# Kernel tuning notes

Hardware: AMD Instinct MI355X
Metric: run time of the kernel (lower is better)

## Reference

```python
import jax, jax.numpy as jnp
import numpy as np

EPS = 1e-5


def setup_inputs() -> dict:
    key = jax.random.key(0)
    ks = jax.random.split(key, 12)
    B, S, M, D, H, dh = 8, 512, 512, 1024, 16, 64
    T = S + M
    w_scale = 0.03  # keep attention logits in a sane range (mimics nn.Linear init scale)
    return {
        "x": jax.random.normal(ks[0], (B, S, D), jnp.float32),
        "mem": jax.random.normal(ks[1], (B, M, D), jnp.float32),
        "R": jax.random.normal(ks[2], (T, D), jnp.float32),
        "u": jax.random.normal(ks[3], (1, H, 1, dh), jnp.float32) * 0.1,
        "t": jax.random.normal(ks[4], (1, H, 1, dh), jnp.float32) * 0.1,
        "Wq": jax.random.normal(ks[5], (H * dh, D), jnp.float32) * w_scale,
        "Wk": jax.random.normal(ks[6], (H * dh, D), jnp.float32) * w_scale,
        "Wv": jax.random.normal(ks[7], (H * dh, D), jnp.float32) * w_scale,
        "Wr": jax.random.normal(ks[8], (H * dh, D), jnp.float32) * w_scale,
        "Wo": jax.random.normal(ks[9], (D, H * dh), jnp.float32) * w_scale,
        "gamma": jnp.ones((D,), jnp.float32),
        "beta": jnp.zeros((D,), jnp.float32),
    }


def reference(x, mem, R, u, t, Wq, Wk, Wv, Wr, Wo, gamma, beta):
    B, S, D = x.shape
    H, dh = u.shape[1], u.shape[3]
    h = jnp.concatenate([mem, x], axis=1)          # [B, T, D]
    T = h.shape[1]
    M = T - S

    q = (x @ Wq.T).reshape(B, S, H, dh).transpose(0, 2, 1, 3)   # [B,H,S,dh]
    k = (h @ Wk.T).reshape(B, T, H, dh).transpose(0, 2, 1, 3)   # [B,H,T,dh]
    v = (h @ Wv.T).reshape(B, T, H, dh).transpose(0, 2, 1, 3)   # [B,H,T,dh]
    r = (R[-T:] @ Wr.T).reshape(1, T, H, dh).transpose(0, 2, 1, 3)  # [1,H,T,dh]

    ac = jnp.einsum("bhid,bhjd->bhij", q + u, k)                # [B,H,S,T]
    bd = jnp.einsum("bhid,hjd->bhij", q + t, r[0])              # [B,H,S,T]

    # circulant shift: shifted[..., i, j] = bd[..., i, (j - i + S - 1) % T]
    idx = (jnp.arange(T)[None, :] - jnp.arange(S)[:, None] + S - 1) % T  # [S,T]
    bd = jnp.take_along_axis(bd, idx[None, None], axis=3)

    # causal mask with memory offset: keep j <= i + M (tril(mem_len)), then
    # exact-zero entries (the masked ones) become -inf, matching the original.
    mask = jnp.arange(T)[None, :] <= (jnp.arange(S)[:, None] + M)        # [S,T]
    score = jnp.where(mask[None, None], (ac + bd) / jnp.sqrt(jnp.float32(dh)), 0.0)
    score = jnp.where(score == 0, -jnp.inf, score)
    p = jax.nn.softmax(score, axis=-1)                                   # [B,H,S,T]

    att = jnp.einsum("bhij,bhjd->bhid", p, v).transpose(0, 2, 1, 3).reshape(B, S, H * dh)
    out = att @ Wo.T                                                      # dropout is identity (p=0/eval)

    y = out + x
    mu = jnp.mean(y, axis=-1, keepdims=True)
    var = jnp.var(y, axis=-1, keepdims=True)
    return (y - mu) / jnp.sqrt(var + EPS) * gamma + beta
```

## Files before the change

### kernel.cpp

```cpp
#include <hip/hip_runtime.h>
#include <math.h>

#define BB 8
#define SS 512
#define MM 512
#define TT 1024
#define DD 1024
#define HH 16
#define DH 64

typedef __attribute__((ext_vector_type(8))) short bf16x8;
typedef __attribute__((ext_vector_type(4))) float f32x4;

#define SCL2E 0.1803368801111f
#define DTHR 11.5f

__device__ __forceinline__ ushort f2bf(float f) {
  union { float f; unsigned u; } x; x.f = f;
  unsigned r = x.u + 0x7fffu + ((x.u >> 16) & 1u);
  return (ushort)(r >> 16);
}
__device__ __forceinline__ float bf2f(ushort u) {
  return __builtin_bit_cast(float, ((unsigned)u) << 16);
}

__device__ __forceinline__ void stage16(void* lds, const void* g) {
  __builtin_amdgcn_global_load_lds((const __attribute__((address_space(1))) void*)g,
                                   (__attribute__((address_space(3))) void*)lds, 16, 0, 0);
}

template <int C>
__device__ __forceinline__ float dppf(float x) {
  return __builtin_bit_cast(float,
      __builtin_amdgcn_update_dpp(0, __builtin_bit_cast(int, x), C, 0xF, 0xF, true));
}
__device__ __forceinline__ float redmax16(float x) {
  x = fmaxf(x, dppf<0xB1>(x));
  x = fmaxf(x, dppf<0x4E>(x));
  x = fmaxf(x, dppf<0x141>(x));
  x = fmaxf(x, dppf<0x140>(x));
  return x;
}
__device__ __forceinline__ float redsum16(float x) {
  x += dppf<0xB1>(x);
  x += dppf<0x4E>(x);
  x += dppf<0x141>(x);
  x += dppf<0x140>(x);
  return x;
}
__device__ __forceinline__ float bperm_f(int byteaddr, float v) {
  return __builtin_bit_cast(float,
      __builtin_amdgcn_ds_bpermute(byteaddr, __builtin_bit_cast(int, v)));
}

__global__ __launch_bounds__(256) void cast_all(
    const float* __restrict__ mem, const float* __restrict__ x,
    const float* __restrict__ R, const float* __restrict__ Wq,
    const float* __restrict__ Wk, const float* __restrict__ Wv,
    const float* __restrict__ Wr, const float* __restrict__ Wo,
    ushort* __restrict__ hb, ushort* __restrict__ Rb, ushort* __restrict__ Wqb,
    ushort* __restrict__ Wkb, ushort* __restrict__ Wvb, ushort* __restrict__ Wrb,
    ushort* __restrict__ Wob) {
  const int M1 = 1 << 20;
  int i = (blockIdx.x * 256 + threadIdx.x) * 8;
  const float* src;
  ushort* dst;
  if (i < 4 * M1) {
    src = mem + i;
    dst = hb + (size_t)i + (size_t)(i >> 19) * 524288;
  } else if (i < 8 * M1) {
    int j = i - 4 * M1;
    src = x + j;
    dst = hb + (size_t)j + (size_t)(j >> 19) * 524288 + 524288;
  } else if (i < 9 * M1) {
    src = R + (i - 8 * M1);  dst = Rb + (i - 8 * M1);
  } else if (i < 10 * M1) {
    src = Wq + (i - 9 * M1); dst = Wqb + (i - 9 * M1);
  } else if (i < 11 * M1) {
    src = Wk + (i - 10 * M1); dst = Wkb + (i - 10 * M1);
  } else if (i < 12 * M1) {
    src = Wv + (i - 11 * M1); dst = Wvb + (i - 11 * M1);
  } else if (i < 13 * M1) {
    src = Wr + (i - 12 * M1); dst = Wrb + (i - 12 * M1);
  } else {
    src = Wo + (i - 13 * M1); dst = Wob + (i - 13 * M1);
  }
  float4 a = *(const float4*)(src);
  float4 c = *(const float4*)(src + 4);
  union { bf16x8 v; ushort u[8]; } pk;
  pk.u[0] = f2bf(a.x); pk.u[1] = f2bf(a.y); pk.u[2] = f2bf(a.z); pk.u[3] = f2bf(a.w);
  pk.u[4] = f2bf(c.x); pk.u[5] = f2bf(c.y); pk.u[6] = f2bf(c.z); pk.u[7] = f2bf(c.w);
  *(bf16x8*)(void*)dst = pk.v;
}

__global__ __launch_bounds__(256, 4) void gemm_qkvr(
    const ushort* __restrict__ hb, const ushort* __restrict__ Rbuf,
    const ushort* __restrict__ Wqb, const ushort* __restrict__ Wkb,
    const ushort* __restrict__ Wvb, const ushort* __restrict__ Wrb,
    ushort* __restrict__ qub,
    ushort* __restrict__ kbo, ushort* __restrict__ vtb, ushort* __restrict__ rbo,
    const float* __restrict__ uvec) {
  __shared__ ushort As0[4096], Bs0[4096], As1[4096], Bs1[4096];
  const int bid = (blockIdx.x & 7) * 168 + (blockIdx.x >> 3);
  const ushort* A;
  const ushort* W;
  ushort* C0 = nullptr;
  bool qadd = false, qslice = false, vmode = false;
  int mt, nx;
  if (bid < 256) {
    mt = bid >> 3; nx = bid & 7;
    A = hb; W = Wqb; C0 = qub; qadd = true; qslice = true;
  } else if (bid < 768) {
    int r = bid - 256; mt = r >> 3; nx = r & 7;
    A = hb; W = Wkb; C0 = kbo;
  } else if (bid < 1280) {
    int r = bid - 768; mt = r >> 3; nx = r & 7;
    A = hb; W = Wvb; C0 = vtb; vmode = true;
  } else {
    int r = bid - 1280; mt = r >> 3; nx = r & 7;
    A = Rbuf; W = Wrb; C0 = rbo;
  }
  const int m0 = mt * 128, n0 = nx * 128;

  const int t = threadIdx.x;
  const int w = t >> 6, l = t & 63;
  const int m16 = l & 15, kg = l >> 4;
  const int wr = w >> 1, wc = w & 1;

  const int c0 = t, c1 = t + 256;
  const int scol = (((t & 3) ^ ((t >> 3) & 3)) * 8);
  const ushort* asrc0;
  const ushort* asrc1;
  {
    int gm0 = m0 + (c0 >> 2), gm1 = m0 + (c1 >> 2);
    if (qslice) {
      asrc0 = A + ((size_t)((gm0 >> 9) * TT + MM + (gm0 & 511))) * DD + scol;
      asrc1 = A + ((size_t)((gm1 >> 9) * TT + MM + (gm1 & 511))) * DD + scol;
    } else {
      asrc0 = A + (size_t)gm0 * DD + scol;
      asrc1 = A + (size_t)gm1 * DD + scol;
    }
  }
  const ushort* bsrc0 = W + (size_t)(n0 + (c0 >> 2)) * DD + scol;
  const ushort* bsrc1 = W + (size_t)(n0 + (c1 >> 2)) * DD + scol;

  const int cbx = ((kg ^ ((m16 >> 1) & 3)) << 3);
  const int arow0 = (wr * 64 + m16) * 32 + cbx;
  const int brow0 = (wc * 64 + m16) * 32 + cbx;

  f32x4 acc[4][4];
#pragma unroll
  for (int mi = 0; mi < 4; ++mi)
#pragma unroll
    for (int ni = 0; ni < 4; ++ni) acc[mi][ni] = (f32x4){0.f, 0.f, 0.f, 0.f};

#define QKVR_STAGE(AS, BS, KOFF)                \
  do {                                          \
    stage16(AS + c0 * 8, asrc0 + (KOFF));       \
    stage16(AS + c1 * 8, asrc1 + (KOFF));       \
    stage16(BS + c0 * 8, bsrc0 + (KOFF));       \
    stage16(BS + c1 * 8, bsrc1 + (KOFF));       \
  } while (0)

#define QKVR_COMPUTE(AS, BS)                                                      \
  do {                                                                            \
    bf16x8 af[4], bfr[4];                                                         \
    _Pragma("unroll") for (int mi = 0; mi < 4; ++mi)                              \
        af[mi] = *(const bf16x8*)(const void*)&AS[arow0 + mi * 512];              \
    _Pragma("unroll") for (int ni = 0; ni < 4; ++ni)                              \
        bfr[ni] = *(const bf16x8*)(const void*)&BS[brow0 + ni * 512];             \
    _Pragma("unroll") for (int mi = 0; mi < 4; ++mi)                              \
        _Pragma("unroll") for (int ni = 0; ni < 4; ++ni)                          \
            acc[mi][ni] = __builtin_amdgcn_mfma_f32_16x16x32_bf16(                \
                af[mi], bfr[ni], acc[mi][ni], 0, 0, 0);                           \
  } while (0)

  QKVR_STAGE(As0, Bs0, 0);

#pragma unroll 1
  for (int kt = 0; kt < 32; kt += 2) {
    QKVR_STAGE(As1, Bs1, (kt + 1) << 5);
    asm volatile("s_waitcnt vmcnt(4)" ::: "memory");
    __builtin_amdgcn_s_barrier();
    QKVR_COMPUTE(As0, Bs0);
    __builtin_amdgcn_s_barrier();
    if (kt + 2 < 32) {
      QKVR_STAGE(As0, Bs0, (kt + 2) << 5);
      asm volatile("s_waitcnt vmcnt(4)" ::: "memory");
    } else {
      asm volatile("s_waitcnt vmcnt(0)" ::: "memory");
    }
    __builtin_amdgcn_s_barrier();
    QKVR_COMPUTE(As1, Bs1);
    __builtin_amdgcn_s_barrier();
  }
#undef QKVR_STAGE
#undef QKVR_COMPUTE

  const int rbase = m0 + wr * 64 + kg * 4;
  const int cbase = n0 + wc * 64 + m16;
  if (vmode) {
    const int bb = m0 >> 10;
    const int tt0 = (m0 & 1023) + wr * 64 + kg * 4;
#pragma unroll
    for (int mi = 0; mi < 4; ++mi)
#pragma unroll
      for (int ni = 0; ni < 4; ++ni) {
        ushort4 o;
        o.x = f2bf(acc[mi][ni][0]); o.y = f2bf(acc[mi][ni][1]);
        o.z = f2bf(acc[mi][ni][2]); o.w = f2bf(acc[mi][ni][3]);
        *(ushort4*)(C0 + ((size_t)(bb * 1024 + cbase + ni * 16) << 10) + tt0 + mi * 16) = o;
      }
  } else if (qadd) {
    float uv[4];
#pragma unroll
    for (int ni = 0; ni < 4; ++ni) uv[ni] = uvec[cbase + ni * 16];
#pragma unroll
    for (int mi = 0; mi < 4; ++mi)
#pragma unroll
      for (int ni = 0; ni < 4; ++ni)
#pragma unroll
        for (int rg = 0; rg < 4; ++rg)
          C0[(size_t)(rbase + mi * 16 + rg) * DD + cbase + ni * 16] = f2bf(acc[mi][ni][rg] + uv[ni]);
  } else {
#pragma unroll
    for (int mi = 0; mi < 4; ++mi)
#pragma unroll
      for (int ni = 0; ni < 4; ++ni)
#pragma unroll
        for (int rg = 0; rg < 4; ++rg)
          C0[(size_t)(rbase + mi * 16 + rg) * DD + cbase + ni * 16] = f2bf(acc[mi][ni][rg]);
  }
}

__global__ __launch_bounds__(256) void gemm_wo(const ushort* __restrict__ A,
                                               const ushort* __restrict__ W,
                                               ushort* __restrict__ Cb) {
  __shared__ ushort As[128 * 32];
  __shared__ ushort Bs[64 * 32];
  const int bid = (blockIdx.x & 7) * 64 + (blockIdx.x >> 3);
  const int mt = bid >> 4, nxt = bid & 15;
  const int m0 = mt * 128, n0 = nxt * 64;
  const int t = threadIdx.x;
  const int w = t >> 6, l = t & 63;
  const int m16 = l & 15, kg = l >> 4;
  const int wr = w >> 1, wc = w & 1;

  const int scol = (((t & 3) ^ ((t >> 3) & 3)) * 8);
  const ushort* asrc0 = A + (size_t)(m0 + (t >> 2)) * DD + scol;
  const ushort* asrc1 = A + (size_t)(m0 + 64 + (t >> 2)) * DD + scol;
  const ushort* bsrc0 = W + (size_t)(n0 + (t >> 2)) * DD + scol;
  ushort* adst0 = As + t * 8;
  ushort* adst1 = As + (t + 256) * 8;
  ushort* bdst0 = Bs + t * 8;

  const int cbx = ((kg ^ ((m16 >> 1) & 3)) << 3);

  f32x4 acc[4][2];
#pragma unroll
  for (int mi = 0; mi < 4; ++mi)
#pragma unroll
    for (int ni = 0; ni < 2; ++ni) acc[mi][ni] = (f32x4){0.f, 0.f, 0.f, 0.f};

  for (int k0 = 0; k0 < DD; k0 += 32) {
    stage16(adst0, asrc0 + k0);
    stage16(adst1, asrc1 + k0);
    stage16(bdst0, bsrc0 + k0);
    __syncthreads();
    bf16x8 af[4], bfr[2];
#pragma unroll
    for (int mi = 0; mi < 4; ++mi)
      af[mi] = *(const bf16x8*)(const void*)&As[(wr * 64 + mi * 16 + m16) * 32 + cbx];
#pragma unroll
    for (int ni = 0; ni < 2; ++ni)
      bfr[ni] = *(const bf16x8*)(const void*)&Bs[(wc * 32 + ni * 16 + m16) * 32 + cbx];
#pragma unroll
    for (int mi = 0; mi < 4; ++mi)
#pragma unroll
      for (int ni = 0; ni < 2; ++ni)
        acc[mi][ni] = __builtin_amdgcn_mfma_f32_16x16x32_bf16(af[mi], bfr[ni], acc[mi][ni], 0, 0, 0);
    __syncthreads();
  }

  const int rbase = m0 + wr * 64 + kg * 4;
  const int cbase = n0 + wc * 32 + m16;
#pragma unroll
  for (int mi = 0; mi < 4; ++mi)
#pragma unroll
    for (int ni = 0; ni < 2; ++ni)
#pragma unroll
      for (int rg = 0; rg < 4; ++rg)
        Cb[(size_t)(rbase + mi * 16 + rg) * DD + cbase + ni * 16] = f2bf(acc[mi][ni][rg]);
}

__global__ __launch_bounds__(256) void attn_mfma(const ushort* __restrict__ qu,
                                                 const ushort* __restrict__ kb,
                                                 const ushort* __restrict__ vt,
                                                 const ushort* __restrict__ rb,
                                                 const float* __restrict__ uvec,
                                                 const float* __restrict__ tvec,
                                                 ushort* __restrict__ att) {
  const int w = threadIdx.x >> 6;
  const int l = threadIdx.x & 63;
  const int m16 = l & 15;
  const int kg = l >> 4;
  const int bid = blockIdx.x;
  const int it = 7 - (bid >> 7);
  const int bh = bid & 127;
  const int b = bh >> 4, h = bh & 15;
  const int i0 = it * 64;

  __shared__ ushort Ks[2][4096];
  __shared__ ushort Vs[4096];
  __shared__ ushort Rl[8192];
  __shared__ ushort plds[4][16][72];

  bf16x8 aqu[2], aqt[2];
  {
    const ushort* qrow = qu + ((size_t)(b * SS + i0 + w * 16 + m16)) * DD + h * DH + kg * 8;
    aqu[0] = *(const bf16x8*)(const void*)(qrow);
    aqu[1] = *(const bf16x8*)(const void*)(qrow + 32);
#pragma unroll
    for (int ks = 0; ks < 2; ++ks) {
      ushort* a = (ushort*)&aqt[ks];
      const ushort* qa = (const ushort*)&aqu[ks];
#pragma unroll
      for (int e = 0; e < 8; ++e) {
        const int col = h * DH + kg * 8 + ks * 32 + e;
        a[e] = f2bf(bf2f(qa[e]) + (tvec[col] - uvec[col]));
      }
    }
  }

  int baddr[4];
  bool bsel[4];
#pragma unroll
  for (int rg = 0; rg < 4; ++rg) {
    const int rw = kg * 4 + rg;
    baddr[rg] = (kg * 16 + ((m16 + 15 - rw) & 15)) << 2;
    bsel[rg] = m16 > rw;
  }

  const int c0 = threadIdx.x, c1 = threadIdx.x + 256;
  const int r0 = c0 >> 3, sc0 = ((c0 & 7) * 8) ^ ((r0 & 7) << 3);
  const int r1 = c1 >> 3, sc1 = ((c1 & 7) * 8) ^ ((r1 & 7) << 3);
  const ushort* kp0 = kb + ((size_t)(b * TT) + r0) * DD + h * DH + sc0;
  const ushort* kp1 = kb + ((size_t)(b * TT) + r1) * DD + h * DH + sc1;
  const ushort* vp0 = vt + ((size_t)(b * 1024 + h * DH + r0)) * 1024 + sc0;
  const ushort* vp1 = vt + ((size_t)(b * 1024 + h * DH + r1)) * 1024 + sc1;

  const int cb0 = (kg * 8) ^ ((m16 & 7) << 3);
  const int cb1 = (kg * 8 + 32) ^ ((m16 & 7) << 3);
  int slot64[5];
#pragma unroll
  for (int f = 0; f < 5; ++f)
    slot64[f] = ((496 - i0 - w * 16 + m16 + f * 16) & 127) << 6;

  {
    const int base0 = 448 - i0;
#pragma unroll
    for (int kk = 0; kk < 4; ++kk) {
      int c = threadIdx.x + kk * 256;
      int ro = c >> 3, cc = c & 7;
      int p = base0 + ro;
      int slot = p & 127;
      stage16(Rl + slot * 64 + cc * 8,
              rb + (size_t)p * DD + h * DH + ((cc * 8) ^ ((ro & 7) << 3)));
    }
  }
  stage16(&Ks[0][c0 * 8], kp0);
  stage16(&Ks[0][c1 * 8], kp1);
  stage16(Vs + c0 * 8, vp0);
  stage16(Vs + c1 * 8, vp1);
  kp0 += (size_t)64 * DD; kp1 += (size_t)64 * DD;
  vp0 += 64; vp1 += 64;

  f32x4 O[4];
  float mrow[4], lrow[4];
#pragma unroll
  for (int nt = 0; nt < 4; ++nt) O[nt] = (f32x4){0.f, 0.f, 0.f, 0.f};
#pragma unroll
  for (int rg = 0; rg < 4; ++rg) { mrow[rg] = -1e30f; lrow[rg] = 0.f; }

  const int ntj = it + 9;
  int cur = 0;
  for (int jt = 0; jt < ntj; ++jt) {
    const int j0 = jt * 64;

    if (jt > 0) {
      stage16(Vs + c0 * 8, vp0);
      stage16(Vs + c1 * 8, vp1);
      vp0 += 64; vp1 += 64;
      const int pstart = 512 + j0 - i0;
#pragma unroll
      for (int kk = 0; kk < 2; ++kk) {
        int c = threadIdx.x + kk * 256;
        int ro = c >> 3, cc = c & 7;
        int p = pstart + ro;
        int pc = p < 1023 ? p : 1023;
        int slot = p & 127;
        stage16(Rl + slot * 64 + cc * 8,
                rb + (size_t)pc * DD + h * DH + ((cc * 8) ^ ((ro & 7) << 3)));
      }
    }
    __syncthreads();

    const ushort* kbase = &Ks[cur][0];
    f32x4 ac[4];
    __builtin_amdgcn_s_setprio(1);
#pragma unroll
    for (int nt = 0; nt < 4; ++nt) {
      ac[nt] = (f32x4){0.f, 0.f, 0.f, 0.f};
      const int row = nt * 16 + m16;
#pragma unroll
      for (int ks = 0; ks < 2; ++ks) {
        bf16x8 bk = *(const bf16x8*)(const void*)(kbase + row * 64 + (ks == 0 ? cb0 : cb1));
        ac[nt] = __builtin_amdgcn_mfma_f32_16x16x32_bf16(aqu[ks], bk, ac[nt], 0, 0, 0);
      }
    }
    __builtin_amdgcn_s_setprio(0);

    if (jt + 1 < ntj) {
      stage16(&Ks[cur ^ 1][c0 * 8], kp0);
      stage16(&Ks[cur ^ 1][c1 * 8], kp1);
      kp0 += (size_t)64 * DD; kp1 += (size_t)64 * DD;
    }

    f32x4 bd[5];
    __builtin_amdgcn_s_setprio(1);
#pragma unroll
    for (int f = 0; f < 5; ++f) {
      f32x4 z = (f32x4){0.f, 0.f, 0.f, 0.f};
      bf16x8 b0 = *(const bf16x8*)(const void*)(Rl + slot64[f] + cb0);
      z = __builtin_amdgcn_mfma_f32_16x16x32_bf16(aqt[0], b0, z, 0, 0, 0);
      bf16x8 b1 = *(const bf16x8*)(const void*)(Rl + slot64[f] + cb1);
      bd[f] = __builtin_amdgcn_mfma_f32_16x16x32_bf16(aqt[1], b1, z, 0, 0, 0);
    }
    __builtin_amdgcn_s_setprio(0);
#pragma unroll
    for (int f = 0; f < 5; ++f) slot64[f] = (slot64[f] + 4096) & 8191;

    float sca[4][4];
#pragma unroll
    for (int rg = 0; rg < 4; ++rg) {
      float rr[5];
#pragma unroll
      for (int f = 0; f < 5; ++f) rr[f] = bperm_f(baddr[rg], bd[f][rg]);
#pragma unroll
      for (int nt = 0; nt < 4; ++nt) {
        float bdv = bsel[rg] ? rr[nt + 1] : rr[nt];
        sca[nt][rg] = (ac[nt][rg] + bdv) * SCL2E;
      }
    }
    if (jt == ntj - 1) {
#pragma unroll
      for (int rg = 0; rg < 4; ++rg) {
        const int jmax = i0 + w * 16 + kg * 4 + rg + MM;
#pragma unroll
        for (int nt = 0; nt < 4; ++nt)
          sca[nt][rg] = (j0 + nt * 16 + m16 <= jmax) ? sca[nt][rg] : -1e30f;
      }
    }

    float pmax[4];
#pragma unroll
    for (int rg = 0; rg < 4; ++rg) {
      float pm = fmaxf(fmaxf(sca[0][rg], sca[1][rg]), fmaxf(sca[2][rg], sca[3][rg]));
      pmax[rg] = redmax16(pm);
    }
    bool grow = false;
#pragma unroll
    for (int rg = 0; rg < 4; ++rg) grow = grow || (pmax[rg] > mrow[rg] + DTHR);
    if (__any(grow)) {
#pragma unroll
      for (int rg = 0; rg < 4; ++rg) {
        float mnew = fmaxf(mrow[rg], pmax[rg]);
        float scale = __builtin_amdgcn_exp2f(mrow[rg] - mnew);
        mrow[rg] = mnew;
        lrow[rg] *= scale;
#pragma unroll
        for (int nt = 0; nt < 4; ++nt) O[nt][rg] *= scale;
      }
    }

#pragma unroll
    for (int rg = 0; rg < 4; ++rg) {
      float ps = 0.f;
#pragma unroll
      for (int nt = 0; nt < 4; ++nt) {
        float p = __builtin_amdgcn_exp2f(sca[nt][rg] - mrow[rg]);
        ps += p;
        plds[w][kg * 4 + rg][nt * 16 + m16] = f2bf(p);
      }
      lrow[rg] += redsum16(ps);
    }

    __builtin_amdgcn_s_setprio(1);
#pragma unroll
    for (int ks = 0; ks < 2; ++ks) {
      bf16x8 pa = *(const bf16x8*)(const void*)&plds[w][m16][kg * 8 + ks * 32];
#pragma unroll
      for (int nt = 0; nt < 4; ++nt) {
        bf16x8 vf = *(const bf16x8*)(const void*)(Vs + (nt * 16 + m16) * 64 + (ks == 0 ? cb0 : cb1));
        O[nt] = __builtin_amdgcn_mfma_f32_16x16x32_bf16(pa, vf, O[nt], 0, 0, 0);
      }
    }
    __builtin_amdgcn_s_setprio(0);

    __syncthreads();
    cur ^= 1;
  }

  float linv[4];
#pragma unroll
  for (int rg = 0; rg < 4; ++rg) linv[rg] = 1.f / lrow[rg];
#pragma unroll
  for (int nt = 0; nt < 4; ++nt) {
#pragma unroll
    for (int rg = 0; rg < 4; ++rg) {
      att[((size_t)(b * SS + i0 + w * 16 + kg * 4 + rg)) * DD + h * DH + nt * 16 + m16] =
          f2bf(O[nt][rg] * linv[rg]);
    }
  }
}

__global__ __launch_bounds__(256) void ln_kernel(const ushort* __restrict__ ypre,
                                                 const ushort* __restrict__ hb,
                                                 const float* __restrict__ gamma,
                                                 const float* __restrict__ beta,
                                                 float* __restrict__ out) {
  const int row = blockIdx.x;
  const int t = threadIdx.x;
  const int lane = t & 63, w = t >> 6;
  const ushort* yr = ypre + (size_t)row * DD;
  const ushort* xr = hb + ((size_t)((row >> 9) * TT + MM + (row & 511))) * DD;

  ushort4 yv = *(const ushort4*)(yr + t * 4);
  ushort4 xv = *(const ushort4*)(xr + t * 4);
  float v0 = bf2f(yv.x) + bf2f(xv.x), v1 = bf2f(yv.y) + bf2f(xv.y);
  float v2 = bf2f(yv.z) + bf2f(xv.z), v3 = bf2f(yv.w) + bf2f(xv.w);

  float s = v0 + v1 + v2 + v3;
  float ss = v0 * v0 + v1 * v1 + v2 * v2 + v3 * v3;
  __shared__ float rs[4], rss[4];
#pragma unroll
  for (int off = 32; off; off >>= 1) {
    s += __shfl_xor(s, off);
    ss += __shfl_xor(ss, off);
  }
  if (!lane) { rs[w] = s; rss[w] = ss; }
  __syncthreads();
  s = rs[0] + rs[1] + rs[2] + rs[3];
  ss = rss[0] + rss[1] + rss[2] + rss[3];
  const float mu = s * (1.f / DD);
  const float var = ss * (1.f / DD) - mu * mu;
  const float rstd = rsqrtf(var + 1e-5f);

  float4 g = *(const float4*)(gamma + t * 4);
  float4 be = *(const float4*)(beta + t * 4);
  float4 o;
  o.x = (v0 - mu) * rstd * g.x + be.x;
  o.y = (v1 - mu) * rstd * g.y + be.y;
  o.z = (v2 - mu) * rstd * g.z + be.z;
  o.w = (v3 - mu) * rstd * g.w + be.w;
  *(float4*)(out + (size_t)row * DD + t * 4) = o;
}

extern "C" void kernel_launch(void* const* d_in, const int* in_sizes, int n_in,
                              void* d_out, int out_size, void* d_ws, size_t ws_size,
                              hipStream_t stream) {
  const float* x = (const float*)d_in[0];
  const float* mem = (const float*)d_in[1];
  const float* R = (const float*)d_in[2];
  const float* u = (const float*)d_in[3];
  const float* tv = (const float*)d_in[4];
  const float* Wq = (const float*)d_in[5];
  const float* Wk = (const float*)d_in[6];
  const float* Wv = (const float*)d_in[7];
  const float* Wr = (const float*)d_in[8];
  const float* Wo = (const float*)d_in[9];
  const float* gamma = (const float*)d_in[10];
  const float* beta = (const float*)d_in[11];
  float* out = (float*)d_out;

  ushort* hb = (ushort*)d_ws;
  ushort* Rb = hb + (8u << 20);
  ushort* Wqb = Rb + (1u << 20);
  ushort* Wkb = Wqb + (1u << 20);
  ushort* Wvb = Wkb + (1u << 20);
  ushort* Wrb = Wvb + (1u << 20);
  ushort* Wob = Wrb + (1u << 20);
  ushort* qu_b = Wob + (1u << 20);
  ushort* kb = qu_b + (4u << 20);
  ushort* vt = kb + (8u << 20);
  ushort* rb = vt + (8u << 20);
  ushort* att = qu_b;
  ushort* ypre = kb;

  dim3 blk(256);

  cast_all<<<dim3(7168), blk, 0, stream>>>(mem, x, R, Wq, Wk, Wv, Wr, Wo,
                                           hb, Rb, Wqb, Wkb, Wvb, Wrb, Wob);

  gemm_qkvr<<<dim3(1344), blk, 0, stream>>>(hb, Rb, Wqb, Wkb, Wvb, Wrb,
                                            qu_b, kb, vt, rb, u);

  attn_mfma<<<dim3(BB * HH * 8), blk, 0, stream>>>(qu_b, kb, vt, rb, u, tv, att);

  gemm_wo<<<dim3(512), blk, 0, stream>>>(att, Wob, ypre);

  ln_kernel<<<dim3(BB * SS), blk, 0, stream>>>(ypre, hb, gamma, beta, out);
}
```

Measured before the change: 162.2 us.

## Double-buffer K, V and R tiles with explicit vmcnt waits in attention

Restructures the attention loop so the K, V and R tiles for the next iteration are all prefetched into a second LDS buffer before the current tile is computed. The loop is unrolled by two to alternate buffers statically. __syncthreads is replaced by raw s_barrier plus a partial s_waitcnt vmcnt, so only the current tile's loads are awaited. The goal is to hide global-load latency behind the MFMA work. The cost is more LDS (V double-buffered, R ring doubled), which may lower occupancy, and correctness now depends on the hand-counted vmcnt value.

```diff
diff --git a/kernel.cpp b/kernel.cpp
--- a/kernel.cpp
+++ b/kernel.cpp
@@ -310,9 +310,9 @@
   const int b = bh >> 4, h = bh & 15;
   const int i0 = it * 64;
 
-  __shared__ ushort Ks[2][4096];
-  __shared__ ushort Vs[4096];
-  __shared__ ushort Rl[8192];
+  __shared__ ushort Ks0[4096], Ks1[4096];
+  __shared__ ushort Vs0[4096], Vs1[4096];
+  __shared__ ushort Rl[16384];
   __shared__ ushort plds[4][16][72];
 
   bf16x8 aqu[2], aqt[2];
@@ -354,7 +354,7 @@
   int slot64[5];
 #pragma unroll
   for (int f = 0; f < 5; ++f)
-    slot64[f] = ((496 - i0 - w * 16 + m16 + f * 16) & 127) << 6;
+    slot64[f] = ((496 - i0 - w * 16 + m16 + f * 16) & 255) << 6;
 
   {
     const int base0 = 448 - i0;
@@ -363,15 +363,15 @@
       int c = threadIdx.x + kk * 256;
       int ro = c >> 3, cc = c & 7;
       int p = base0 + ro;
-      int slot = p & 127;
+      int slot = p & 255;
       stage16(Rl + slot * 64 + cc * 8,
               rb + (size_t)p * DD + h * DH + ((cc * 8) ^ ((ro & 7) << 3)));
     }
   }
-  stage16(&Ks[0][c0 * 8], kp0);
-  stage16(&Ks[0][c1 * 8], kp1);
-  stage16(Vs + c0 * 8, vp0);
-  stage16(Vs + c1 * 8, vp1);
+  stage16(Ks0 + c0 * 8, kp0);
+  stage16(Ks0 + c1 * 8, kp1);
+  stage16(Vs0 + c0 * 8, vp0);
+  stage16(Vs0 + c1 * 8, vp1);
   kp0 += (size_t)64 * DD; kp1 += (size_t)64 * DD;
   vp0 += 64; vp1 += 64;
 
@@ -383,29 +383,29 @@
   for (int rg = 0; rg < 4; ++rg) { mrow[rg] = -1e30f; lrow[rg] = 0.f; }
 
   const int ntj = it + 9;
-  int cur = 0;
-  for (int jt = 0; jt < ntj; ++jt) {
+
+  auto stage_next = [&](ushort* KN, ushort* VN, int jt) {
+    stage16(KN + c0 * 8, kp0);
+    stage16(KN + c1 * 8, kp1);
+    kp0 += (size_t)64 * DD; kp1 += (size_t)64 * DD;
+    stage16(VN + c0 * 8, vp0);
+    stage16(VN + c1 * 8, vp1);
+    vp0 += 64; vp1 += 64;
+    const int pstart = 576 + jt * 64 - i0;
+#pragma unroll
+    for (int kk = 0; kk < 2; ++kk) {
+      int c = threadIdx.x + kk * 256;
+      int ro = c >> 3, cc = c & 7;
+      int p = pstart + ro;
+      int pc = p < 1023 ? p : 1023;
+      int slot = p & 255;
+      stage16(Rl + slot * 64 + cc * 8,
+              rb + (size_t)pc * DD + h * DH + ((cc * 8) ^ ((ro & 7) << 3)));
+    }
+  };
+
+  auto compute_tile = [&](const ushort* kbase, const ushort* vbase, int jt) {
     const int j0 = jt * 64;
-
-    if (jt > 0) {
-      stage16(Vs + c0 * 8, vp0);
-      stage16(Vs + c1 * 8, vp1);
-      vp0 += 64; vp1 += 64;
-      const int pstart = 512 + j0 - i0;
-#pragma unroll
-      for (int kk = 0; kk < 2; ++kk) {
-        int c = threadIdx.x + kk * 256;
-        int ro = c >> 3, cc = c & 7;
-        int p = pstart + ro;
-        int pc = p < 1023 ? p : 1023;
-        int slot = p & 127;
-        stage16(Rl + slot * 64 + cc * 8,
-                rb + (size_t)pc * DD + h * DH + ((cc * 8) ^ ((ro & 7) << 3)));
-      }
-    }
-    __syncthreads();
-
-    const ushort* kbase = &Ks[cur][0];
     f32x4 ac[4];
     __builtin_amdgcn_s_setprio(1);
 #pragma unroll
@@ -418,16 +418,7 @@
         ac[nt] = __builtin_amdgcn_mfma_f32_16x16x32_bf16(aqu[ks], bk, ac[nt], 0, 0, 0);
       }
     }
-    __builtin_amdgcn_s_setprio(0);
-
-    if (jt + 1 < ntj) {
-      stage16(&Ks[cur ^ 1][c0 * 8], kp0);
-      stage16(&Ks[cur ^ 1][c1 * 8], kp1);
-      kp0 += (size_t)64 * DD; kp1 += (size_t)64 * DD;
-    }
-
     f32x4 bd[5];
-    __builtin_amdgcn_s_setprio(1);
 #pragma unroll
     for (int f = 0; f < 5; ++f) {
       f32x4 z = (f32x4){0.f, 0.f, 0.f, 0.f};
@@ -438,7 +429,7 @@
     }
     __builtin_amdgcn_s_setprio(0);
 #pragma unroll
-    for (int f = 0; f < 5; ++f) slot64[f] = (slot64[f] + 4096) & 8191;
+    for (int f = 0; f < 5; ++f) slot64[f] = (slot64[f] + 4096) & 16383;
 
     float sca[4][4];
 #pragma unroll
@@ -501,14 +492,41 @@
       bf16x8 pa = *(const bf16x8*)(const void*)&plds[w][m16][kg * 8 + ks * 32];
 #pragma unroll
       for (int nt = 0; nt < 4; ++nt) {
-        bf16x8 vf = *(const bf16x8*)(const void*)(Vs + (nt * 16 + m16) * 64 + (ks == 0 ? cb0 : cb1));
+        bf16x8 vf = *(const bf16x8*)(const void*)(vbase + (nt * 16 + m16) * 64 + (ks == 0 ? cb0 : cb1));
         O[nt] = __builtin_amdgcn_mfma_f32_16x16x32_bf16(pa, vf, O[nt], 0, 0, 0);
       }
     }
     __builtin_amdgcn_s_setprio(0);
-
-    __syncthreads();
-    cur ^= 1;
+  };
+
+  int jt = 0;
+  for (;;) {
+    {
+      if (jt + 1 < ntj) {
+        stage_next(Ks1, Vs1, jt);
+        asm volatile("s_waitcnt vmcnt(6)" ::: "memory");
+      } else {
+        asm volatile("s_waitcnt vmcnt(0)" ::: "memory");
+      }
+      __builtin_amdgcn_s_barrier();
+      compute_tile(Ks0, Vs0, jt);
+      if (jt + 1 == ntj) break;
+      __builtin_amdgcn_s_barrier();
+      ++jt;
+    }
+    {
+      if (jt + 1 < ntj) {
+        stage_next(Ks0, Vs0, jt);
+        asm volatile("s_waitcnt vmcnt(6)" ::: "memory");
+      } else {
+        asm volatile("s_waitcnt vmcnt(0)" ::: "memory");
+      }
+      __builtin_amdgcn_s_barrier();
+      compute_tile(Ks1, Vs1, jt);
+      if (jt + 1 == ntj) break;
+      __builtin_amdgcn_s_barrier();
+      ++jt;
+    }
   }
 
   float linv[4];
```

New measurement: 158.3 us. 2.4% less time.
